# Kernel tuning notes

Measured on AMD Instinct MI355X. Metric: run time of the kernel, lower is better.

The kernel has to match this reference:

```python
import jax, jax.numpy as jnp
import numpy as np

TEMPERATURE = 0.1
N, D = 8192, 1024

def setup_inputs() -> dict:
    key = jax.random.key(0)
    k1, k2 = jax.random.split(key)
    im = jax.random.normal(k1, (N, D), dtype=jnp.float32)
    cap = jax.random.normal(k2, (N, D), dtype=jnp.float32)
    return {"im": im, "cap": cap}

def reference(im, cap):
    # InfoNCE (info_nce package) L2-normalizes query, positive and negatives.
    # Per-sample loop: for image i, positive = cap[i], negatives = cap[j != i].
    # Logits set = sim(im_i, cap_j) for all j, positive at j == i, so
    # loss_i = logsumexp_j(S[i, j] / T) - S[i, i] / T  (CLIP-style CE).
    imn = im / jnp.linalg.norm(im, axis=-1, keepdims=True)
    capn = cap / jnp.linalg.norm(cap, axis=-1, keepdims=True)
    S = jnp.einsum('id,jd->ij', imn, capn) / TEMPERATURE  # [N, N]
    diag = jnp.diagonal(S)
    loss_i2c = jax.nn.logsumexp(S, axis=1) - diag  # image -> caption direction
    loss_c2i = jax.nn.logsumexp(S, axis=0) - diag  # caption -> image direction
    # original averages all 2N per-sample losses
    return 0.5 * (jnp.mean(loss_i2c) + jnp.mean(loss_c2i))
```

## Files before the change

### kernel.cpp

```cpp
#include <hip/hip_runtime.h>
#include <stdint.h>

#define N_ 8192
#define D_ 1024
#define EPILOGUE_SCALE (10.0f / 256.0f)
#define ENC_SCALE 16.0f
#define CHUNK 524288

typedef float f32x4 __attribute__((ext_vector_type(4)));
typedef float f32x16 __attribute__((ext_vector_type(16)));
typedef int i32x4 __attribute__((ext_vector_type(4)));
typedef int i32x8 __attribute__((ext_vector_type(8)));

#define GLD16(gsrc, ldst)                                                    \
  __builtin_amdgcn_global_load_lds(                                          \
      (const __attribute__((address_space(1))) unsigned int*)(gsrc),         \
      (__attribute__((address_space(3))) unsigned int*)(ldst), 16, 0, 0)


__global__ __launch_bounds__(1024) void normalize_k(
    const float* __restrict__ im, const float* __restrict__ cap,
    unsigned int* __restrict__ imn, unsigned int* __restrict__ capn,
    float* __restrict__ diag, float* __restrict__ sums ) {
  __shared__ unsigned int ldsA[16 * 260];
  __shared__ unsigned int ldsB[16 * 260];
  const int til = blockIdx.x;
  const int t = threadIdx.x;
  if (til < 4) ((float4*)sums)[til * 1024 + t] = (float4){0.f, 0.f, 0.f, 0.f};

  const int r = t >> 6, j = t & 63;
  const int row = til * 16 + r;
  const float4* __restrict__ aR = (const float4*)(im + (size_t)row * D_);
  const float4* __restrict__ bR = (const float4*)(cap + (size_t)row * D_);

  float4 a0 = aR[j], a1 = aR[j + 64], a2 = aR[j + 128], a3 = aR[j + 192];
  float4 b0 = bR[j], b1 = bR[j + 64], b2 = bR[j + 128], b3 = bR[j + 192];

  float ssa = a0.x * a0.x + a0.y * a0.y + a0.z * a0.z + a0.w * a0.w
            + a1.x * a1.x + a1.y * a1.y + a1.z * a1.z + a1.w * a1.w
            + a2.x * a2.x + a2.y * a2.y + a2.z * a2.z + a2.w * a2.w
            + a3.x * a3.x + a3.y * a3.y + a3.z * a3.z + a3.w * a3.w;
  float ssb = b0.x * b0.x + b0.y * b0.y + b0.z * b0.z + b0.w * b0.w
            + b1.x * b1.x + b1.y * b1.y + b1.z * b1.z + b1.w * b1.w
            + b2.x * b2.x + b2.y * b2.y + b2.z * b2.z + b2.w * b2.w
            + b3.x * b3.x + b3.y * b3.y + b3.z * b3.z + b3.w * b3.w;
  float dt  = a0.x * b0.x + a0.y * b0.y + a0.z * b0.z + a0.w * b0.w
            + a1.x * b1.x + a1.y * b1.y + a1.z * b1.z + a1.w * b1.w
            + a2.x * b2.x + a2.y * b2.y + a2.z * b2.z + a2.w * b2.w
            + a3.x * b3.x + a3.y * b3.y + a3.z * b3.z + a3.w * b3.w;
#pragma unroll
  for (int o = 1; o < 64; o <<= 1) {
    ssa += __shfl_xor(ssa, o, 64);
    ssb += __shfl_xor(ssb, o, 64);
    dt  += __shfl_xor(dt, o, 64);
  }
  const float ra = rsqrtf(ssa), rb = rsqrtf(ssb);
  if (j == 0) diag[row] = dt * ra * rb * 10.0f;
  const float sa = ra * ENC_SCALE, sb = rb * ENC_SCALE;

#define CVT_ST(av, bv, ofs)                                                  \
  {                                                                          \
    int pa_ = __builtin_amdgcn_cvt_pk_fp8_f32(av.x * sa, av.y * sa, 0, false); \
    pa_ = __builtin_amdgcn_cvt_pk_fp8_f32(av.z * sa, av.w * sa, pa_, true);  \
    int pb_ = __builtin_amdgcn_cvt_pk_fp8_f32(bv.x * sb, bv.y * sb, 0, false); \
    pb_ = __builtin_amdgcn_cvt_pk_fp8_f32(bv.z * sb, bv.w * sb, pb_, true);  \
    ldsA[r * 260 + j + (ofs)] = (unsigned int)pa_;                           \
    ldsB[r * 260 + j + (ofs)] = (unsigned int)pb_;                           \
  }
  CVT_ST(a0, b0, 0)
  CVT_ST(a1, b1, 64)
  CVT_ST(a2, b2, 128)
  CVT_ST(a3, b3, 192)
#undef CVT_ST
  __syncthreads();

  {
    const int q = t >> 4, rp = t & 15;
    const uint4 va = *(const uint4*)&ldsA[rp * 260 + q * 4];
    const uint4 vb = *(const uint4*)&ldsB[rp * 260 + q * 4];
    const int row32 = ((til & 1) << 4) + rp;
    const size_t d = (size_t)(q >> 2) * CHUNK + (size_t)(til >> 1) * 2048
                   + (size_t)((q & 1) << 10)
                   + (size_t)((((q >> 1) & 1) << 5) + row32) * 16;
    *(uint4*)((unsigned char*)imn + d) = va;
    *(uint4*)((unsigned char*)capn + d) = vb;
  }
}

__global__ __launch_bounds__(256, 2) void gemm_lse_k(
    const unsigned char* __restrict__ A,
    const unsigned char* __restrict__ B,
    float* __restrict__ rowsum, float* __restrict__ colsum) {
  __shared__ unsigned char lds[2][8192];
  const int t = threadIdx.x;
  const int w = t >> 6, l = t & 63;
  const int l16 = l * 16;

  const int bid = blockIdx.x + (blockIdx.y << 6);
  const int nid = (bid & 7) * 256 + (bid >> 3);
  const int rowT = ((nid >> 8) << 3) + (nid & 7);
  const int colT = (nid >> 3) & 31;

  const size_t baseA = (size_t)rowT * 8192;
  const size_t baseB = (size_t)colT * 16384;

  const unsigned char* __restrict__ srcA0 = A + baseA + w * 2048 + l16;
  const unsigned char* __restrict__ srcA1 = srcA0 + 1024;
  const int ofsA0 = w * 2048, ofsA1 = ofsA0 + 1024;

  const unsigned char* __restrict__ srcB = B + baseB + w * 4096 + l16;

#define STAGE(kc, buf)                                                       \
  {                                                                          \
    const size_t kofs = (size_t)(kc) * CHUNK;                                \
    GLD16(srcA0 + kofs, &lds[buf][ofsA0]);                                   \
    GLD16(srcA1 + kofs, &lds[buf][ofsA1]);                                   \
  }

#define BLOAD(dst, kc)                                                       \
  {                                                                          \
    const unsigned char* bp = srcB + (size_t)(kc) * CHUNK;                   \
    dst[0] = *(const i32x4*)(bp);                                            \
    dst[1] = *(const i32x4*)(bp + 1024);                                     \
    dst[2] = *(const i32x4*)(bp + 2048);                                     \
    dst[3] = *(const i32x4*)(bp + 3072);                                     \
  }

  f32x16 acc[4][2];
#pragma unroll
  for (int m = 0; m < 4; ++m)
#pragma unroll
    for (int n = 0; n < 2; ++n)
#pragma unroll
      for (int r = 0; r < 16; ++r) acc[m][n][r] = 0.f;

  i32x4 bb0[4], bb1[4];

#define COMPUTE(buf, bset)                                                   \
  {                                                                          \
    const unsigned char* Lc = &lds[buf][0];                                  \
    i32x8 a_[4], b_[2];                                                      \
    _Pragma("unroll")                                                        \
    for (int m = 0; m < 4; ++m) {                                            \
      i32x4 lo = *(const i32x4*)(Lc + m * 2048 + l16);                       \
      i32x4 hi = *(const i32x4*)(Lc + m * 2048 + 1024 + l16);                \
      a_[m] = __builtin_shufflevector(lo, hi, 0, 1, 2, 3, 4, 5, 6, 7);       \
    }                                                                        \
    b_[0] = __builtin_shufflevector(bset[0], bset[1], 0, 1, 2, 3, 4, 5, 6, 7); \
    b_[1] = __builtin_shufflevector(bset[2], bset[3], 0, 1, 2, 3, 4, 5, 6, 7); \
    _Pragma("unroll")                                                        \
    for (int m = 0; m < 4; ++m)                                              \
      _Pragma("unroll")                                                      \
      for (int n = 0; n < 2; ++n)                                            \
        acc[m][n] = __builtin_amdgcn_mfma_scale_f32_32x32x64_f8f6f4(         \
            a_[m], b_[n], acc[m][n], 0, 0, 0, 0x7F7F7F7F, 0, 0x7F7F7F7F);    \
  }

  STAGE(0, 0)
  BLOAD(bb0, 0)

#pragma unroll 1
  for (int kt = 0; kt < 14; kt += 2) {
    STAGE(kt + 1, (kt + 1) & 1)
    BLOAD(bb1, kt + 1)
    asm volatile("s_waitcnt vmcnt(6)" ::: "memory");
    __builtin_amdgcn_s_barrier();
    COMPUTE(kt & 1, bb0)
    __builtin_amdgcn_s_barrier();
    STAGE(kt + 2, (kt + 2) & 1)
    BLOAD(bb0, kt + 2)
    asm volatile("s_waitcnt vmcnt(6)" ::: "memory");
    __builtin_amdgcn_s_barrier();
    COMPUTE((kt + 1) & 1, bb1)
    __builtin_amdgcn_s_barrier();
  }
  STAGE(15, 1)
  BLOAD(bb1, 15)
  asm volatile("s_waitcnt vmcnt(6)" ::: "memory");
  __builtin_amdgcn_s_barrier();
  COMPUTE(0, bb0)
  __builtin_amdgcn_s_barrier();
  asm volatile("s_waitcnt vmcnt(0)" ::: "memory");
  __builtin_amdgcn_s_barrier();
  COMPUTE(1, bb1)
#undef COMPUTE
#undef BLOAD
#undef STAGE

#pragma unroll
  for (int m = 0; m < 4; ++m)
#pragma unroll
    for (int n = 0; n < 2; ++n)
#pragma unroll
      for (int r = 0; r < 16; ++r)
        acc[m][n][r] = __expf(acc[m][n][r] * EPILOGUE_SCALE);

  const int rowBase = rowT * 128;
  const int colBase = colT * 256 + w * 64;
#pragma unroll
  for (int m = 0; m < 4; ++m) {
    f32x16 s = acc[m][0] + acc[m][1];
#pragma unroll
    for (int r = 0; r < 16; ++r) {
      float v = s[r];
      v += __shfl_xor(v, 1, 64);
      v += __shfl_xor(v, 2, 64);
      v += __shfl_xor(v, 4, 64);
      v += __shfl_xor(v, 8, 64);
      v += __shfl_xor(v, 16, 64);
      if ((l & 31) == 0)
        atomicAdd(&rowsum[rowBase + m * 32 + (r & 3) + 8 * (r >> 2) + 4 * (l >> 5)], v);
    }
  }
#pragma unroll
  for (int n = 0; n < 2; ++n) {
    float v = 0.f;
#pragma unroll
    for (int r = 0; r < 16; ++r) v += acc[0][n][r] + acc[1][n][r]
                                    + acc[2][n][r] + acc[3][n][r];
    v += __shfl_xor(v, 32, 64);
    if (l < 32)
      atomicAdd(&colsum[colBase + n * 32 + l], v);
  }
}

__global__ __launch_bounds__(256) void finalize_k(
    const float* __restrict__ rowsum, const float* __restrict__ colsum,
    const float* __restrict__ diag, float* __restrict__ out) {
  const int t = threadIdx.x;
  float lse = 0.f, dg = 0.f;
  for (int i = t; i < N_; i += 256) {
    lse += __logf(rowsum[i]) + __logf(colsum[i]);
    dg += diag[i];
  }
#pragma unroll
  for (int o = 32; o > 0; o >>= 1) {
    lse += __shfl_down(lse, o, 64);
    dg  += __shfl_down(dg, o, 64);
  }
  __shared__ float red[2][4];
  const int w = t >> 6, l = t & 63;
  if (l == 0) { red[0][w] = lse; red[1][w] = dg; }
  __syncthreads();
  if (t == 0) {
    lse = red[0][0] + red[0][1] + red[0][2] + red[0][3];
    dg  = red[1][0] + red[1][1] + red[1][2] + red[1][3];
    out[0] = 0.5f * lse / (float)N_ - dg / (float)N_;
  }
}

extern "C" void kernel_launch(void* const* d_in, const int* in_sizes, int n_in,
                              void* d_out, int out_size, void* d_ws, size_t ws_size,
                              hipStream_t stream) {
  const float* im = (const float*)d_in[0];
  const float* cap = (const float*)d_in[1];
  float* out = (float*)d_out;
  char* ws = (char*)d_ws;
  unsigned char* imn = (unsigned char*)ws;
  unsigned char* capn = imn + (size_t)N_ * D_;
  float* rowsum = (float*)(ws + 2 * (size_t)N_ * D_);
  float* colsum = rowsum + N_;
  float* diag = colsum + N_;

  normalize_k<<<512, 1024, 0, stream>>>(im, cap, (unsigned int*)imn,
                                        (unsigned int*)capn, diag, rowsum);
  gemm_lse_k<<<dim3(64, 32), 256, 0, stream>>>(imn, capn, rowsum, colsum);
  finalize_k<<<1, 256, 0, stream>>>(rowsum, colsum, diag, out);
}
```

Baseline: 206.1 us.

## Shrink GEMM tile to 128x128 with 2x2 wave grid and 3 blocks/CU

Changes the GEMM block tile from 128x256 to 128x128, arranges the four waves as a 2x2 grid of 64x64 sub-tiles, and doubles the grid to 64x64 blocks. The caption operand is re-laid out by the normalize kernel so each lane can load a full 32-byte B fragment in one i32x8 load. Launch bounds rise to 3 blocks per CU. The aim is better occupancy and latency hiding from fewer accumulators per wave, at the cost of less reuse per block, more global traffic, and twice as many epilogue atomics.

```diff
diff --git a/kernel.cpp b/kernel.cpp
--- a/kernel.cpp
+++ b/kernel.cpp
@@ -79,15 +79,16 @@
     const uint4 va = *(const uint4*)&ldsA[rp * 260 + q * 4];
     const uint4 vb = *(const uint4*)&ldsB[rp * 260 + q * 4];
     const int row32 = ((til & 1) << 4) + rp;
-    const size_t d = (size_t)(q >> 2) * CHUNK + (size_t)(til >> 1) * 2048
-                   + (size_t)((q & 1) << 10)
-                   + (size_t)((((q >> 1) & 1) << 5) + row32) * 16;
-    *(uint4*)((unsigned char*)imn + d) = va;
-    *(uint4*)((unsigned char*)capn + d) = vb;
-  }
-}
-
-__global__ __launch_bounds__(256, 2) void gemm_lse_k(
+    const int slot = (((q >> 1) & 1) << 5) + row32;
+    const size_t base = (size_t)(q >> 2) * CHUNK + (size_t)(til >> 1) * 2048;
+    const size_t dA = base + (size_t)((q & 1) << 10) + (size_t)slot * 16;
+    const size_t dB = base + (size_t)slot * 32 + (size_t)((q & 1) << 4);
+    *(uint4*)((unsigned char*)imn + dA) = va;
+    *(uint4*)((unsigned char*)capn + dB) = vb;
+  }
+}
+
+__global__ __launch_bounds__(256, 3) void gemm_lse_k(
     const unsigned char* __restrict__ A,
     const unsigned char* __restrict__ B,
     float* __restrict__ rowsum, float* __restrict__ colsum) {
@@ -97,63 +98,58 @@
   const int l16 = l * 16;
 
   const int bid = blockIdx.x + (blockIdx.y << 6);
-  const int nid = (bid & 7) * 256 + (bid >> 3);
-  const int rowT = ((nid >> 8) << 3) + (nid & 7);
-  const int colT = (nid >> 3) & 31;
+  const int nid = (bid & 7) * 512 + (bid >> 3);
+  const int rowT = ((nid >> 9) << 3) + (nid & 7);
+  const int colT = (nid >> 3) & 63;
 
   const size_t baseA = (size_t)rowT * 8192;
-  const size_t baseB = (size_t)colT * 16384;
-
-  const unsigned char* __restrict__ srcA0 = A + baseA + w * 2048 + l16;
-  const unsigned char* __restrict__ srcA1 = srcA0 + 1024;
-  const int ofsA0 = w * 2048, ofsA1 = ofsA0 + 1024;
-
-  const unsigned char* __restrict__ srcB = B + baseB + w * 4096 + l16;
+  const size_t baseB = (size_t)colT * 8192;
+
+  const int wr = w >> 1, wc = w & 1;
+
+  const unsigned char* __restrict__ srcA = A + baseA + t * 16;
+  const unsigned char* __restrict__ srcB = B + baseB + wc * 4096 + l * 32;
 
 #define STAGE(kc, buf)                                                       \
   {                                                                          \
-    const size_t kofs = (size_t)(kc) * CHUNK;                                \
-    GLD16(srcA0 + kofs, &lds[buf][ofsA0]);                                   \
-    GLD16(srcA1 + kofs, &lds[buf][ofsA1]);                                   \
+    const unsigned char* ap = srcA + (size_t)(kc) * CHUNK;                   \
+    GLD16(ap, &lds[buf][t * 16]);                                            \
+    GLD16(ap + 4096, &lds[buf][4096 + t * 16]);                              \
   }
 
 #define BLOAD(dst, kc)                                                       \
   {                                                                          \
     const unsigned char* bp = srcB + (size_t)(kc) * CHUNK;                   \
-    dst[0] = *(const i32x4*)(bp);                                            \
-    dst[1] = *(const i32x4*)(bp + 1024);                                     \
-    dst[2] = *(const i32x4*)(bp + 2048);                                     \
-    dst[3] = *(const i32x4*)(bp + 3072);                                     \
-  }
-
-  f32x16 acc[4][2];
-#pragma unroll
-  for (int m = 0; m < 4; ++m)
+    dst[0] = *(const i32x8*)(bp);                                            \
+    dst[1] = *(const i32x8*)(bp + 2048);                                     \
+  }
+
+  f32x16 acc[2][2];
+#pragma unroll
+  for (int m = 0; m < 2; ++m)
 #pragma unroll
     for (int n = 0; n < 2; ++n)
 #pragma unroll
       for (int r = 0; r < 16; ++r) acc[m][n][r] = 0.f;
 
-  i32x4 bb0[4], bb1[4];
+  i32x8 bb0[2], bb1[2];
 
 #define COMPUTE(buf, bset)                                                   \
   {                                                                          \
     const unsigned char* Lc = &lds[buf][0];                                  \
-    i32x8 a_[4], b_[2];                                                      \
+    i32x8 a_[2];                                                             \
     _Pragma("unroll")                                                        \
-    for (int m = 0; m < 4; ++m) {                                            \
-      i32x4 lo = *(const i32x4*)(Lc + m * 2048 + l16);                       \
-      i32x4 hi = *(const i32x4*)(Lc + m * 2048 + 1024 + l16);                \
+    for (int m = 0; m < 2; ++m) {                                            \
+      i32x4 lo = *(const i32x4*)(Lc + (wr * 2 + m) * 2048 + l16);            \
+      i32x4 hi = *(const i32x4*)(Lc + (wr * 2 + m) * 2048 + 1024 + l16);     \
       a_[m] = __builtin_shufflevector(lo, hi, 0, 1, 2, 3, 4, 5, 6, 7);       \
     }                                                                        \
-    b_[0] = __builtin_shufflevector(bset[0], bset[1], 0, 1, 2, 3, 4, 5, 6, 7); \
-    b_[1] = __builtin_shufflevector(bset[2], bset[3], 0, 1, 2, 3, 4, 5, 6, 7); \
     _Pragma("unroll")                                                        \
-    for (int m = 0; m < 4; ++m)                                              \
+    for (int m = 0; m < 2; ++m)                                              \
       _Pragma("unroll")                                                      \
       for (int n = 0; n < 2; ++n)                                            \
         acc[m][n] = __builtin_amdgcn_mfma_scale_f32_32x32x64_f8f6f4(         \
-            a_[m], b_[n], acc[m][n], 0, 0, 0, 0x7F7F7F7F, 0, 0x7F7F7F7F);    \
+            a_[m], bset[n], acc[m][n], 0, 0, 0, 0x7F7F7F7F, 0, 0x7F7F7F7F);  \
   }
 
   STAGE(0, 0)
@@ -161,17 +157,17 @@
 
 #pragma unroll 1
   for (int kt = 0; kt < 14; kt += 2) {
-    STAGE(kt + 1, (kt + 1) & 1)
+    STAGE(kt + 1, 1)
     BLOAD(bb1, kt + 1)
     asm volatile("s_waitcnt vmcnt(6)" ::: "memory");
     __builtin_amdgcn_s_barrier();
-    COMPUTE(kt & 1, bb0)
-    __builtin_amdgcn_s_barrier();
-    STAGE(kt + 2, (kt + 2) & 1)
+    COMPUTE(0, bb0)
+    __builtin_amdgcn_s_barrier();
+    STAGE(kt + 2, 0)
     BLOAD(bb0, kt + 2)
     asm volatile("s_waitcnt vmcnt(6)" ::: "memory");
     __builtin_amdgcn_s_barrier();
-    COMPUTE((kt + 1) & 1, bb1)
+    COMPUTE(1, bb1)
     __builtin_amdgcn_s_barrier();
   }
   STAGE(15, 1)
@@ -188,17 +184,17 @@
 #undef STAGE
 
 #pragma unroll
-  for (int m = 0; m < 4; ++m)
+  for (int m = 0; m < 2; ++m)
 #pragma unroll
     for (int n = 0; n < 2; ++n)
 #pragma unroll
       for (int r = 0; r < 16; ++r)
         acc[m][n][r] = __expf(acc[m][n][r] * EPILOGUE_SCALE);
 
-  const int rowBase = rowT * 128;
-  const int colBase = colT * 256 + w * 64;
-#pragma unroll
-  for (int m = 0; m < 4; ++m) {
+  const int rowBase = rowT * 128 + wr * 64;
+  const int colBase = colT * 128 + wc * 64;
+#pragma unroll
+  for (int m = 0; m < 2; ++m) {
     f32x16 s = acc[m][0] + acc[m][1];
 #pragma unroll
     for (int r = 0; r < 16; ++r) {
@@ -216,8 +212,7 @@
   for (int n = 0; n < 2; ++n) {
     float v = 0.f;
 #pragma unroll
-    for (int r = 0; r < 16; ++r) v += acc[0][n][r] + acc[1][n][r]
-                                    + acc[2][n][r] + acc[3][n][r];
+    for (int r = 0; r < 16; ++r) v += acc[0][n][r] + acc[1][n][r];
     v += __shfl_xor(v, 32, 64);
     if (l < 32)
       atomicAdd(&colsum[colBase + n * 32 + l], v);
@@ -264,6 +259,6 @@
 
   normalize_k<<<512, 1024, 0, stream>>>(im, cap, (unsigned int*)imn,
                                         (unsigned int*)capn, diag, rowsum);
-  gemm_lse_k<<<dim3(64, 32), 256, 0, stream>>>(imn, capn, rowsum, colsum);
+  gemm_lse_k<<<dim3(64, 64), 256, 0, stream>>>(imn, capn, rowsum, colsum);
   finalize_k<<<1, 256, 0, stream>>>(rowsum, colsum, diag, out);
 }
```

After: 203.1 us. About the same (-1.4%).
